# Kernel tuning notes

Hardware: AMD Instinct MI355X
Metric: run time of the kernel (lower is better)

## Reference

```python
import jax, jax.numpy as jnp
import numpy as np

NV = 20000; NC = 20000; E = 500000
IN_SHAPE = 2; PE_DIM = 8; HID = 64; NL = 3
EPS = 1e-7  # GENConv message eps


def _lin(x, w, b):
    return x @ w + b


def _encode(x, pe, ew, eb, pw1, pb1, pw2, pb2):
    # relu(cat([Linear(x), 0.5*(pe_mlp(pe)+pe_mlp(-pe))], dim=1))
    def pe_mlp(p):
        return _lin(jax.nn.relu(_lin(p, pw1, pb1)), pw2, pb2)
    h = jnp.concatenate([_lin(x, ew, eb), 0.5 * (pe_mlp(pe) + pe_mlp(-pe))], axis=1)
    return jax.nn.relu(h)


def _genconv(x_src, x_dst, src, dst, ewt, lew, leb, w1, b1, w2, b2, n_dst):
    # GENConv(aggr='softmax', t=1, norm=None, msg_norm=False, edge_dim=1)
    msg = jax.nn.relu(x_src[src] + _lin(ewt, lew, leb)) + EPS  # [E, HID]
    m = jax.ops.segment_max(msg, dst, num_segments=n_dst)      # stable segment softmax
    ex = jnp.exp(msg - m[dst])
    s = jax.ops.segment_sum(ex, dst, num_segments=n_dst)
    agg = jax.ops.segment_sum(ex / (s[dst] + 1e-16) * msg, dst, num_segments=n_dst)
    out = agg + x_dst
    return _lin(jax.nn.relu(_lin(out, w1, b1)), w2, b2)  # MLP [hid -> 2hid -> hid]


def setup_inputs() -> dict:
    key = jax.random.key(0)
    ks = iter(jax.random.split(key, 64))
    d = {}
    d['x_vals'] = jax.random.normal(next(ks), (NV, IN_SHAPE), jnp.float32)
    d['x_cons'] = jax.random.normal(next(ks), (NC, IN_SHAPE), jnp.float32)
    d['pe_vals'] = jax.random.normal(next(ks), (NV, PE_DIM), jnp.float32)
    d['pe_cons'] = jax.random.normal(next(ks), (NC, PE_DIM), jnp.float32)
    d['edge_index_v2c'] = jnp.stack([
        jax.random.randint(next(ks), (E,), 0, NV),
        jax.random.randint(next(ks), (E,), 0, NC)])
    d['edge_index_c2v'] = jnp.stack([
        jax.random.randint(next(ks), (E,), 0, NC),
        jax.random.randint(next(ks), (E,), 0, NV)])
    d['edge_weight_v2c'] = jax.random.normal(next(ks), (E, 1), jnp.float32)
    d['edge_weight_c2v'] = jax.random.normal(next(ks), (E, 1), jnp.float32)
    def p(shape):
        return jax.random.normal(next(ks), shape, jnp.float32) * 0.05
    for k_ in ['vals', 'cons']:
        d[f'enc_{k_}_w'] = p((IN_SHAPE, HID // 2)); d[f'enc_{k_}_b'] = p((HID // 2,))
        d[f'pe_{k_}_w1'] = p((PE_DIM, HID)); d[f'pe_{k_}_b1'] = p((HID,))
        d[f'pe_{k_}_w2'] = p((HID, HID // 2)); d[f'pe_{k_}_b2'] = p((HID // 2,))
    for c in ['v2c', 'c2v']:
        d[f'{c}_edge_w'] = p((NL, 1, HID)); d[f'{c}_edge_b'] = p((NL, HID))
        d[f'{c}_w1'] = p((NL, HID, 2 * HID)); d[f'{c}_b1'] = p((NL, 2 * HID))
        d[f'{c}_w2'] = p((NL, 2 * HID, HID)); d[f'{c}_b2'] = p((NL, HID))
    for k_ in ['vals', 'cons']:
        d[f'pred_{k_}_w1'] = p((HID, HID)); d[f'pred_{k_}_b1'] = p((HID,))
        d[f'pred_{k_}_w2'] = p((HID, 1)); d[f'pred_{k_}_b2'] = p((1,))
    return d


def reference(x_vals, x_cons, pe_vals, pe_cons, edge_index_v2c, edge_index_c2v,
              edge_weight_v2c, edge_weight_c2v,
              enc_vals_w, enc_vals_b, pe_vals_w1, pe_vals_b1, pe_vals_w2, pe_vals_b2,
              enc_cons_w, enc_cons_b, pe_cons_w1, pe_cons_b1, pe_cons_w2, pe_cons_b2,
              v2c_edge_w, v2c_edge_b, v2c_w1, v2c_b1, v2c_w2, v2c_b2,
              c2v_edge_w, c2v_edge_b, c2v_w1, c2v_b1, c2v_w2, c2v_b2,
              pred_vals_w1, pred_vals_b1, pred_vals_w2, pred_vals_b2,
              pred_cons_w1, pred_cons_b1, pred_cons_w2, pred_cons_b2):
    vals = _encode(x_vals, pe_vals, enc_vals_w, enc_vals_b,
                   pe_vals_w1, pe_vals_b1, pe_vals_w2, pe_vals_b2)
    cons = _encode(x_cons, pe_cons, enc_cons_w, enc_cons_b,
                   pe_cons_w1, pe_cons_b1, pe_cons_w2, pe_cons_b2)
    hv, hc = [], []
    for i in range(NL):
        cons = _genconv(vals, cons, edge_index_v2c[0], edge_index_v2c[1],
                        edge_weight_v2c, v2c_edge_w[i], v2c_edge_b[i],
                        v2c_w1[i], v2c_b1[i], v2c_w2[i], v2c_b2[i], NC)
        vals = _genconv(cons, vals, edge_index_c2v[0], edge_index_c2v[1],
                        edge_weight_c2v, c2v_edge_w[i], c2v_edge_b[i],
                        c2v_w1[i], c2v_b1[i], c2v_w2[i], c2v_b2[i], NV)
        hc.append(cons); hv.append(vals)
    V = jnp.stack(hv)  # [NL, NV, HID]
    C = jnp.stack(hc)  # [NL, NC, HID]
    pv = _lin(jax.nn.relu(_lin(V, pred_vals_w1, pred_vals_b1)), pred_vals_w2, pred_vals_b2)
    pc = _lin(jax.nn.relu(_lin(C, pred_cons_w1, pred_cons_b1)), pred_cons_w2, pred_cons_b2)
    return pv[..., 0].T, pc[..., 0].T  # [NV, NL], [NC, NL]
```

## Files before the change

### kernel.cpp

```cpp
#include <hip/hip_runtime.h>
#include <hip/hip_fp16.h>

#define NVN 20000
#define NCN 20000
#define NE  500000
#define HID 64
#define NLAYER 3
#define TN 40
#define BSH 8
#define NB 79
#define CAPSH 14
#define CAP (1 << CAPSH)
#define NBCAP (NB * CAP)
#define P1E 2048

__device__ __forceinline__ float relu_(float x) { return fmaxf(x, 0.0f); }

__global__ __launch_bounds__(256) void bininit_kernel(
    int* __restrict__ bincurA, int* __restrict__ bincurB)
{
    int t = threadIdx.x;
    if (t < NB) { bincurA[t] = t << CAPSH; bincurB[t] = t << CAPSH; }
}

__global__ __launch_bounds__(256) void scatter_p1_kernel(
    const int* __restrict__ eiA, const float* __restrict__ ewA,
    int* __restrict__ bincurA, int2* __restrict__ stageA,
    const int* __restrict__ eiB, const float* __restrict__ ewB,
    int* __restrict__ bincurB, int2* __restrict__ stageB)
{
    __shared__ int rnk[P1E];
    __shared__ int cnt[NB], base_[NB];
    int t = threadIdx.x;
    int e0 = blockIdx.x * P1E;

    for (int g = 0; g < 2; ++g) {
        const int* ei   = g ? eiB : eiA;
        const float* ew = g ? ewB : ewA;
        int* bincur     = g ? bincurB : bincurA;
        int2* stage     = g ? stageB : stageA;

        if (t < NB) cnt[t] = 0;
        __syncthreads();
        for (int i = t; i < P1E; i += 256) {
            int e = e0 + i;
            if (e < NE) {
                int d = ei[NE + e];
                rnk[i] = atomicAdd(&cnt[d >> BSH], 1);
            }
        }
        __syncthreads();
        if (t < NB && cnt[t] > 0) base_[t] = atomicAdd(&bincur[t], cnt[t]);
        __syncthreads();
        for (int i = t; i < P1E; i += 256) {
            int e = e0 + i;
            if (e < NE) {
                int s = ei[e], d = ei[NE + e];
                float w = ew[e];
                stage[base_[d >> BSH] + rnk[i]] =
                    make_int2((int)((unsigned)s | ((unsigned)d << 16)), __float_as_int(w));
            }
        }
        __syncthreads();
    }
}

__global__ __launch_bounds__(1024) void scatter_p2_kernel(
    const int* __restrict__ bincurA, const int2* __restrict__ stageA,
    int* __restrict__ rowptrA, int* __restrict__ rowendA, int2* __restrict__ pairA,
    const int* __restrict__ bincurB, const int2* __restrict__ stageB,
    int* __restrict__ rowptrB, int* __restrict__ rowendB, int2* __restrict__ pairB)
{
    __shared__ int deg[256], pfx[256], cur[256];
    int g = blockIdx.x / NB;
    int b = blockIdx.x % NB;
    const int* bincur  = g ? bincurB : bincurA;
    const int2* stage  = g ? stageB : stageA;
    int* rowptr        = g ? rowptrB : rowptrA;
    int* rowend        = g ? rowendB : rowendA;
    int2* pair         = g ? pairB : pairA;

    int d0 = b << BSH;
    int d1 = min(d0 + 256, NCN);
    int nd = d1 - d0;
    int t = threadIdx.x;
    int estart = b << CAPSH;
    int eend = bincur[b];

    if (t < 256) deg[t] = 0;
    __syncthreads();
    for (int e = estart + t; e < eend; e += 1024) {
        int dst = (int)((unsigned)stage[e].x >> 16);
        atomicAdd(&deg[dst - d0], 1);
    }
    __syncthreads();
    if (t < 256) pfx[t] = deg[t];
    __syncthreads();
    for (int off = 1; off < 256; off <<= 1) {
        int v = (t >= off && t < 256) ? pfx[t - off] : 0;
        __syncthreads();
        if (t < 256) pfx[t] += v;
        __syncthreads();
    }
    if (t < nd) {
        int ex = estart + pfx[t] - deg[t];
        rowptr[d0 + t] = ex;
        rowend[d0 + t] = estart + pfx[t];
        cur[t] = ex;
    }
    __syncthreads();
    for (int e = estart + t; e < eend; e += 1024) {
        int2 s = stage[e];
        unsigned u = (unsigned)s.x;
        int src = (int)(u & 0xFFFFu);
        int dst = (int)(u >> 16);
        int p = atomicAdd(&cur[dst - d0], 1);
        pair[p] = make_int2(src, s.y);
    }
}

__global__ __launch_bounds__(256) void encode2_kernel(
    const float* __restrict__ xv, const float* __restrict__ pev,
    const float* __restrict__ ewv, const float* __restrict__ ebv,
    const float* __restrict__ pw1v, const float* __restrict__ pb1v,
    const float* __restrict__ pw2v, const float* __restrict__ pb2v,
    const float* __restrict__ xc, const float* __restrict__ pec,
    const float* __restrict__ ewc, const float* __restrict__ ebc,
    const float* __restrict__ pw1c, const float* __restrict__ pb1c,
    const float* __restrict__ pw2c, const float* __restrict__ pb2c,
    float* __restrict__ outv, float* __restrict__ outc,
    __half* __restrict__ outv16, __half* __restrict__ outc16)
{
    __shared__ float sh[4][64];
    const int VB = (NVN + 3) / 4;
    int wave = threadIdx.x >> 6, lane = threadIdx.x & 63;
    int b = blockIdx.x;
    bool isC = (b >= VB);
    const float* x   = isC ? xc : xv;
    const float* pe  = isC ? pec : pev;
    const float* ew  = isC ? ewc : ewv;
    const float* eb  = isC ? ebc : ebv;
    const float* pw1 = isC ? pw1c : pw1v;
    const float* pb1 = isC ? pb1c : pb1v;
    const float* pw2 = isC ? pw2c : pw2v;
    const float* pb2 = isC ? pb2c : pb2v;
    float* out = isC ? outc : outv;
    __half* out16 = isC ? outc16 : outv16;
    int N = isC ? NCN : NVN;
    int n = (isC ? b - VB : b) * 4 + wave;
    if (n >= N) return;

    float accp = pb1[lane], accm = accp;
#pragma unroll
    for (int k = 0; k < 8; ++k) {
        float p = pe[n * 8 + k];
        float w = pw1[k * 64 + lane];
        accp += p * w;
        accm -= p * w;
    }
    float hs = 0.5f * (relu_(accp) + relu_(accm));
    float* my = sh[wave];
    my[lane] = hs;
    __builtin_amdgcn_wave_barrier();

    int col = lane & 31;
    float peo = pb2[col];
#pragma unroll
    for (int k = 0; k < 64; k += 4) {
        float4 hv = *(const float4*)(my + k);
        peo = fmaf(hv.x, pw2[(k + 0) * 32 + col], peo);
        peo = fmaf(hv.y, pw2[(k + 1) * 32 + col], peo);
        peo = fmaf(hv.z, pw2[(k + 2) * 32 + col], peo);
        peo = fmaf(hv.w, pw2[(k + 3) * 32 + col], peo);
    }
    float lino = x[n * 2 + 0] * ew[col] + x[n * 2 + 1] * ew[32 + col] + eb[col];
    float h = (lane < 32) ? lino : peo;
    float r = relu_(h);
    out[n * 64 + lane] = r;
    out16[n * 64 + lane] = __float2half(r);
}

__global__ __launch_bounds__(256, 8) void edge_agg_kernel(
    const __half* __restrict__ xsrc,
    const float* __restrict__ xdst,
    const int* __restrict__ rowptr,
    const int* __restrict__ rowend,
    const int2* __restrict__ pair,
    const float* __restrict__ lew,
    const float* __restrict__ leb,
    float* __restrict__ oa,
    int N)
{
    int wave = threadIdx.x >> 6, lane = threadIdx.x & 63;
    int n = blockIdx.x * 4 + wave;
    if (n >= N) return;

    int start = __builtin_amdgcn_readfirstlane(rowptr[n]);
    int end   = __builtin_amdgcn_readfirstlane(rowend[n]);
    float lw = lew[lane], lb = leb[lane];
    float xd = xdst[(size_t)n * 64 + lane];

    float den = 0.0f, num = 0.0f;
    int j = start;

    if (j + 8 <= end) {
        int2 pb[8];
#pragma unroll
        for (int c = 0; c < 8; ++c) pb[c] = pair[j + c];

        for (; j + 16 <= end; j += 8) {
            float xv[8];
#pragma unroll
            for (int c = 0; c < 8; ++c)
                xv[c] = __half2float(xsrc[(size_t)pb[c].x * 64 + lane]);
            int2 pn[8];
#pragma unroll
            for (int c = 0; c < 8; ++c) pn[c] = pair[j + 8 + c];
#pragma unroll
            for (int c = 0; c < 8; ++c) {
                float msg = relu_(fmaf(__int_as_float(pb[c].y), lw, xv[c] + lb)) + 1e-7f;
                float e = __expf(msg);
                den += e;
                num = fmaf(e, msg, num);
            }
#pragma unroll
            for (int c = 0; c < 8; ++c) pb[c] = pn[c];
        }
        {
            float xv[8];
#pragma unroll
            for (int c = 0; c < 8; ++c)
                xv[c] = __half2float(xsrc[(size_t)pb[c].x * 64 + lane]);
#pragma unroll
            for (int c = 0; c < 8; ++c) {
                float msg = relu_(fmaf(__int_as_float(pb[c].y), lw, xv[c] + lb)) + 1e-7f;
                float e = __expf(msg);
                den += e;
                num = fmaf(e, msg, num);
            }
            j += 8;
        }
    }
    for (; j < end; ++j) {
        int2 p = pair[j];
        float xv = __half2float(xsrc[(size_t)p.x * 64 + lane]);
        float msg = relu_(fmaf(__int_as_float(p.y), lw, xv + lb)) + 1e-7f;
        float e = __expf(msg);
        den += e;
        num = fmaf(e, msg, num);
    }

    oa[(size_t)n * 64 + lane] = num / (den + 1e-16f) + xd;
}

__global__ __launch_bounds__(256, 4) void mlp_kernel(
    const float* __restrict__ oa,
    float* __restrict__ feat,
    __half* __restrict__ feat16,
    const float* __restrict__ w1,
    const float* __restrict__ b1,
    const float* __restrict__ w2,
    const float* __restrict__ b2,
    const float* __restrict__ pw1,
    const float* __restrict__ pb1,
    const float* __restrict__ pw2,
    const float* __restrict__ pb2,
    float* __restrict__ outp,
    int N, int layer)
{
    __shared__ float act[TN][68];
    __shared__ float hid[TN][132];
    __shared__ float b1s[128];
    __shared__ float b2s[64];
    __shared__ float pb1s[64];
    __shared__ float pw2s[64];

    int tid = threadIdx.x;
    if (tid < 128) b1s[tid] = b1[tid];
    if (tid < 64) { b2s[tid] = b2[tid]; pb1s[tid] = pb1[tid]; pw2s[tid] = pw2[tid]; }
    float pb2v = pb2[0];

    int o4 = (tid & 31) * 4;
    int o2 = (tid & 31) * 2;
    int n5 = (tid >> 5) * 5;
    __syncthreads();

    int ntiles = N / TN;
    for (int tile = blockIdx.x; tile < ntiles; tile += gridDim.x) {
        int base = tile * TN;
        {
            const float4* g4 = (const float4*)(oa + (size_t)base * 64);
            for (int i = tid; i < TN * 16; i += 256)
                *(float4*)&act[i >> 4][(i & 15) * 4] = g4[i];
        }
        __syncthreads();

        {
            float acc[5][4];
#pragma unroll
            for (int i = 0; i < 5; ++i)
#pragma unroll
                for (int q = 0; q < 4; ++q) acc[i][q] = b1s[o4 + q];
#pragma unroll 2
            for (int k = 0; k < 64; k += 4) {
                float4 a[5];
#pragma unroll
                for (int i = 0; i < 5; ++i) a[i] = *(const float4*)&act[n5 + i][k];
                float4 w0 = *(const float4*)&w1[(k + 0) * 128 + o4];
                float4 wq1 = *(const float4*)&w1[(k + 1) * 128 + o4];
                float4 wq2 = *(const float4*)&w1[(k + 2) * 128 + o4];
                float4 wq3 = *(const float4*)&w1[(k + 3) * 128 + o4];
#pragma unroll
                for (int i = 0; i < 5; ++i) {
                    acc[i][0] = fmaf(a[i].x, w0.x, acc[i][0]);
                    acc[i][1] = fmaf(a[i].x, w0.y, acc[i][1]);
                    acc[i][2] = fmaf(a[i].x, w0.z, acc[i][2]);
                    acc[i][3] = fmaf(a[i].x, w0.w, acc[i][3]);
                    acc[i][0] = fmaf(a[i].y, wq1.x, acc[i][0]);
                    acc[i][1] = fmaf(a[i].y, wq1.y, acc[i][1]);
                    acc[i][2] = fmaf(a[i].y, wq1.z, acc[i][2]);
                    acc[i][3] = fmaf(a[i].y, wq1.w, acc[i][3]);
                    acc[i][0] = fmaf(a[i].z, wq2.x, acc[i][0]);
                    acc[i][1] = fmaf(a[i].z, wq2.y, acc[i][1]);
                    acc[i][2] = fmaf(a[i].z, wq2.z, acc[i][2]);
                    acc[i][3] = fmaf(a[i].z, wq2.w, acc[i][3]);
                    acc[i][0] = fmaf(a[i].w, wq3.x, acc[i][0]);
                    acc[i][1] = fmaf(a[i].w, wq3.y, acc[i][1]);
                    acc[i][2] = fmaf(a[i].w, wq3.z, acc[i][2]);
                    acc[i][3] = fmaf(a[i].w, wq3.w, acc[i][3]);
                }
            }
#pragma unroll
            for (int i = 0; i < 5; ++i) {
                float4 h4 = make_float4(relu_(acc[i][0]), relu_(acc[i][1]),
                                        relu_(acc[i][2]), relu_(acc[i][3]));
                *(float4*)&hid[n5 + i][o4] = h4;
            }
        }
        __syncthreads();

        {
            float acc[5][2];
#pragma unroll
            for (int i = 0; i < 5; ++i) { acc[i][0] = b2s[o2]; acc[i][1] = b2s[o2 + 1]; }
#pragma unroll 2
            for (int k = 0; k < 128; k += 4) {
                float4 a[5];
#pragma unroll
                for (int i = 0; i < 5; ++i) a[i] = *(const float4*)&hid[n5 + i][k];
                float2 w0 = *(const float2*)&w2[(k + 0) * 64 + o2];
                float2 wq1 = *(const float2*)&w2[(k + 1) * 64 + o2];
                float2 wq2 = *(const float2*)&w2[(k + 2) * 64 + o2];
                float2 wq3 = *(const float2*)&w2[(k + 3) * 64 + o2];
#pragma unroll
                for (int i = 0; i < 5; ++i) {
                    acc[i][0] = fmaf(a[i].x, w0.x, acc[i][0]);
                    acc[i][1] = fmaf(a[i].x, w0.y, acc[i][1]);
                    acc[i][0] = fmaf(a[i].y, wq1.x, acc[i][0]);
                    acc[i][1] = fmaf(a[i].y, wq1.y, acc[i][1]);
                    acc[i][0] = fmaf(a[i].z, wq2.x, acc[i][0]);
                    acc[i][1] = fmaf(a[i].z, wq2.y, acc[i][1]);
                    acc[i][0] = fmaf(a[i].w, wq3.x, acc[i][0]);
                    acc[i][1] = fmaf(a[i].w, wq3.y, acc[i][1]);
                }
            }
#pragma unroll
            for (int i = 0; i < 5; ++i) {
                float2 r2 = make_float2(acc[i][0], acc[i][1]);
                *(float2*)&feat[(size_t)(base + n5 + i) * 64 + o2] = r2;
                *(__half2*)&feat16[(size_t)(base + n5 + i) * 64 + o2] =
                    __floats2half2_rn(r2.x, r2.y);
                *(float2*)&act[n5 + i][o2] = r2;
            }
        }
        __syncthreads();

        {
            float acc[5][2];
#pragma unroll
            for (int i = 0; i < 5; ++i) { acc[i][0] = pb1s[o2]; acc[i][1] = pb1s[o2 + 1]; }
#pragma unroll 2
            for (int k = 0; k < 64; k += 4) {
                float4 a[5];
#pragma unroll
                for (int i = 0; i < 5; ++i) a[i] = *(const float4*)&act[n5 + i][k];
                float2 w0 = *(const float2*)&pw1[(k + 0) * 64 + o2];
                float2 wq1 = *(const float2*)&pw1[(k + 1) * 64 + o2];
                float2 wq2 = *(const float2*)&pw1[(k + 2) * 64 + o2];
                float2 wq3 = *(const float2*)&pw1[(k + 3) * 64 + o2];
#pragma unroll
                for (int i = 0; i < 5; ++i) {
                    acc[i][0] = fmaf(a[i].x, w0.x, acc[i][0]);
                    acc[i][1] = fmaf(a[i].x, w0.y, acc[i][1]);
                    acc[i][0] = fmaf(a[i].y, wq1.x, acc[i][0]);
                    acc[i][1] = fmaf(a[i].y, wq1.y, acc[i][1]);
                    acc[i][0] = fmaf(a[i].z, wq2.x, acc[i][0]);
                    acc[i][1] = fmaf(a[i].z, wq2.y, acc[i][1]);
                    acc[i][0] = fmaf(a[i].w, wq3.x, acc[i][0]);
                    acc[i][1] = fmaf(a[i].w, wq3.y, acc[i][1]);
                }
            }
            float pw2a = pw2s[o2], pw2b = pw2s[o2 + 1];
            float ps[5];
#pragma unroll
            for (int i = 0; i < 5; ++i)
                ps[i] = relu_(acc[i][0]) * pw2a + relu_(acc[i][1]) * pw2b;
#pragma unroll
            for (int msk = 16; msk >= 1; msk >>= 1) {
#pragma unroll
                for (int i = 0; i < 5; ++i)
                    ps[i] += __shfl_xor(ps[i], msk, 64);
            }
            if ((tid & 31) == 0) {
#pragma unroll
                for (int i = 0; i < 5; ++i)
                    outp[(size_t)(base + n5 + i) * NLAYER + layer] = ps[i] + pb2v;
            }
        }
        __syncthreads();
    }
}

extern "C" void kernel_launch(void* const* d_in, const int* in_sizes, int n_in,
                              void* d_out, int out_size, void* d_ws, size_t ws_size,
                              hipStream_t stream)
{
    const float* x_vals   = (const float*)d_in[0];
    const float* x_cons   = (const float*)d_in[1];
    const float* pe_vals  = (const float*)d_in[2];
    const float* pe_cons  = (const float*)d_in[3];
    const int*   ei_v2c   = (const int*)d_in[4];
    const int*   ei_c2v   = (const int*)d_in[5];
    const float* ew_v2c   = (const float*)d_in[6];
    const float* ew_c2v   = (const float*)d_in[7];
    const float* enc_vals_w = (const float*)d_in[8];
    const float* enc_vals_b = (const float*)d_in[9];
    const float* pe_vals_w1 = (const float*)d_in[10];
    const float* pe_vals_b1 = (const float*)d_in[11];
    const float* pe_vals_w2 = (const float*)d_in[12];
    const float* pe_vals_b2 = (const float*)d_in[13];
    const float* enc_cons_w = (const float*)d_in[14];
    const float* enc_cons_b = (const float*)d_in[15];
    const float* pe_cons_w1 = (const float*)d_in[16];
    const float* pe_cons_b1 = (const float*)d_in[17];
    const float* pe_cons_w2 = (const float*)d_in[18];
    const float* pe_cons_b2 = (const float*)d_in[19];
    const float* v2c_edge_w = (const float*)d_in[20];
    const float* v2c_edge_b = (const float*)d_in[21];
    const float* v2c_w1     = (const float*)d_in[22];
    const float* v2c_b1     = (const float*)d_in[23];
    const float* v2c_w2     = (const float*)d_in[24];
    const float* v2c_b2     = (const float*)d_in[25];
    const float* c2v_edge_w = (const float*)d_in[26];
    const float* c2v_edge_b = (const float*)d_in[27];
    const float* c2v_w1     = (const float*)d_in[28];
    const float* c2v_b1     = (const float*)d_in[29];
    const float* c2v_w2     = (const float*)d_in[30];
    const float* c2v_b2     = (const float*)d_in[31];
    const float* pred_vals_w1 = (const float*)d_in[32];
    const float* pred_vals_b1 = (const float*)d_in[33];
    const float* pred_vals_w2 = (const float*)d_in[34];
    const float* pred_vals_b2 = (const float*)d_in[35];
    const float* pred_cons_w1 = (const float*)d_in[36];
    const float* pred_cons_b1 = (const float*)d_in[37];
    const float* pred_cons_w2 = (const float*)d_in[38];
    const float* pred_cons_b2 = (const float*)d_in[39];

    float* out = (float*)d_out;
    float* out_c = out + (size_t)NVN * NLAYER;

    const size_t NF = (size_t)NVN * 64;

    float* ws     = (float*)d_ws;
    float* feat_v = ws;
    float* feat_c = feat_v + NF;
    float* oa     = feat_c + NF;
    int2* v2c_pair  = (int2*)(oa + NF);
    int2* c2v_pair  = v2c_pair + NBCAP;
    int2* v2c_stage = c2v_pair + NBCAP;
    int2* c2v_stage = v2c_stage + NBCAP;
    __half* feat16_v = (__half*)(c2v_stage + NBCAP);
    __half* feat16_c = feat16_v + NF;
    int* ip = (int*)(feat16_c + NF);
    int* v2c_bincur  = ip; ip += NB;
    int* c2v_bincur  = ip; ip += NB;
    int* v2c_rowptr  = ip; ip += NCN;
    int* v2c_rowend  = ip; ip += NCN;
    int* c2v_rowptr  = ip; ip += NVN;
    int* c2v_rowend  = ip; ip += NVN;

    const int p1b = (NE + P1E - 1) / P1E;

    bininit_kernel<<<1, 256, 0, stream>>>(v2c_bincur, c2v_bincur);
    scatter_p1_kernel<<<p1b, 256, 0, stream>>>(
        ei_v2c, ew_v2c, v2c_bincur, v2c_stage,
        ei_c2v, ew_c2v, c2v_bincur, c2v_stage);
    scatter_p2_kernel<<<2 * NB, 1024, 0, stream>>>(
        v2c_bincur, v2c_stage, v2c_rowptr, v2c_rowend, v2c_pair,
        c2v_bincur, c2v_stage, c2v_rowptr, c2v_rowend, c2v_pair);

    encode2_kernel<<<(NVN + 3) / 4 + (NCN + 3) / 4, 256, 0, stream>>>(
        x_vals, pe_vals, enc_vals_w, enc_vals_b,
        pe_vals_w1, pe_vals_b1, pe_vals_w2, pe_vals_b2,
        x_cons, pe_cons, enc_cons_w, enc_cons_b,
        pe_cons_w1, pe_cons_b1, pe_cons_w2, pe_cons_b2,
        feat_v, feat_c, feat16_v, feat16_c);

    for (int i = 0; i < NLAYER; ++i) {
        edge_agg_kernel<<<(NCN + 3) / 4, 256, 0, stream>>>(
            feat16_v, feat_c, v2c_rowptr, v2c_rowend, v2c_pair,
            v2c_edge_w + (size_t)i * HID, v2c_edge_b + (size_t)i * HID,
            oa, NCN);
        mlp_kernel<<<NCN / TN, 256, 0, stream>>>(
            oa, feat_c, feat16_c,
            v2c_w1 + (size_t)i * 8192, v2c_b1 + (size_t)i * 128,
            v2c_w2 + (size_t)i * 8192, v2c_b2 + (size_t)i * 64,
            pred_cons_w1, pred_cons_b1, pred_cons_w2, pred_cons_b2,
            out_c, NCN, i);
        edge_agg_kernel<<<(NVN + 3) / 4, 256, 0, stream>>>(
            feat16_c, feat_v, c2v_rowptr, c2v_rowend, c2v_pair,
            c2v_edge_w + (size_t)i * HID, c2v_edge_b + (size_t)i * HID,
            oa, NVN);
        mlp_kernel<<<NVN / TN, 256, 0, stream>>>(
            oa, feat_v, feat16_v,
            c2v_w1 + (size_t)i * 8192, c2v_b1 + (size_t)i * 128,
            c2v_w2 + (size_t)i * 8192, c2v_b2 + (size_t)i * 64,
            pred_vals_w1, pred_vals_b1, pred_vals_w2, pred_vals_b2,
            out, NVN, i);
    }
}
```

Measured before the change: 426.0 us.

## Fuse edge softmax aggregation with node MLP into a single kernel

Each block now aggregates the incoming edges of 8 destination nodes, keeps the aggregated rows in shared memory, and runs the two-layer MLP plus the prediction head on them in the same kernel. This removes the global round trip through the intermediate `oa` buffer and halves the number of kernel launches per layer. In exchange, the MLP tile shrinks from 40 to 8 nodes, so each weight element is reused across fewer rows and more weight traffic goes through the caches.

```diff
diff --git a/kernel.cpp b/kernel.cpp
--- a/kernel.cpp
+++ b/kernel.cpp
@@ -6,7 +6,7 @@
 #define NE  500000
 #define HID 64
 #define NLAYER 3
-#define TN 40
+#define TN 8
 #define BSH 8
 #define NB 79
 #define CAPSH 14
@@ -180,7 +180,7 @@
     out16[n * 64 + lane] = __float2half(r);
 }
 
-__global__ __launch_bounds__(256, 8) void edge_agg_kernel(
+__global__ __launch_bounds__(256, 8) void fused_kernel(
     const __half* __restrict__ xsrc,
     const float* __restrict__ xdst,
     const int* __restrict__ rowptr,
@@ -188,73 +188,6 @@
     const int2* __restrict__ pair,
     const float* __restrict__ lew,
     const float* __restrict__ leb,
-    float* __restrict__ oa,
-    int N)
-{
-    int wave = threadIdx.x >> 6, lane = threadIdx.x & 63;
-    int n = blockIdx.x * 4 + wave;
-    if (n >= N) return;
-
-    int start = __builtin_amdgcn_readfirstlane(rowptr[n]);
-    int end   = __builtin_amdgcn_readfirstlane(rowend[n]);
-    float lw = lew[lane], lb = leb[lane];
-    float xd = xdst[(size_t)n * 64 + lane];
-
-    float den = 0.0f, num = 0.0f;
-    int j = start;
-
-    if (j + 8 <= end) {
-        int2 pb[8];
-#pragma unroll
-        for (int c = 0; c < 8; ++c) pb[c] = pair[j + c];
-
-        for (; j + 16 <= end; j += 8) {
-            float xv[8];
-#pragma unroll
-            for (int c = 0; c < 8; ++c)
-                xv[c] = __half2float(xsrc[(size_t)pb[c].x * 64 + lane]);
-            int2 pn[8];
-#pragma unroll
-            for (int c = 0; c < 8; ++c) pn[c] = pair[j + 8 + c];
-#pragma unroll
-            for (int c = 0; c < 8; ++c) {
-                float msg = relu_(fmaf(__int_as_float(pb[c].y), lw, xv[c] + lb)) + 1e-7f;
-                float e = __expf(msg);
-                den += e;
-                num = fmaf(e, msg, num);
-            }
-#pragma unroll
-            for (int c = 0; c < 8; ++c) pb[c] = pn[c];
-        }
-        {
-            float xv[8];
-#pragma unroll
-            for (int c = 0; c < 8; ++c)
-                xv[c] = __half2float(xsrc[(size_t)pb[c].x * 64 + lane]);
-#pragma unroll
-            for (int c = 0; c < 8; ++c) {
-                float msg = relu_(fmaf(__int_as_float(pb[c].y), lw, xv[c] + lb)) + 1e-7f;
-                float e = __expf(msg);
-                den += e;
-                num = fmaf(e, msg, num);
-            }
-            j += 8;
-        }
-    }
-    for (; j < end; ++j) {
-        int2 p = pair[j];
-        float xv = __half2float(xsrc[(size_t)p.x * 64 + lane]);
-        float msg = relu_(fmaf(__int_as_float(p.y), lw, xv + lb)) + 1e-7f;
-        float e = __expf(msg);
-        den += e;
-        num = fmaf(e, msg, num);
-    }
-
-    oa[(size_t)n * 64 + lane] = num / (den + 1e-16f) + xd;
-}
-
-__global__ __launch_bounds__(256, 4) void mlp_kernel(
-    const float* __restrict__ oa,
     float* __restrict__ feat,
     __half* __restrict__ feat16,
     const float* __restrict__ w1,
@@ -270,154 +203,163 @@
 {
     __shared__ float act[TN][68];
     __shared__ float hid[TN][132];
-    __shared__ float b1s[128];
-    __shared__ float b2s[64];
-    __shared__ float pb1s[64];
-    __shared__ float pw2s[64];
 
     int tid = threadIdx.x;
-    if (tid < 128) b1s[tid] = b1[tid];
-    if (tid < 64) { b2s[tid] = b2[tid]; pb1s[tid] = pb1[tid]; pw2s[tid] = pw2[tid]; }
-    float pb2v = pb2[0];
+    int wave = tid >> 6, lane = tid & 63;
+    int base = blockIdx.x * TN;
+
+    {
+        float lw = lew[lane], lb = leb[lane];
+#pragma unroll
+        for (int q = 0; q < 2; ++q) {
+            int row = wave * 2 + q;
+            int n = base + row;
+            int start = __builtin_amdgcn_readfirstlane(rowptr[n]);
+            int end   = __builtin_amdgcn_readfirstlane(rowend[n]);
+            float xd = xdst[(size_t)n * 64 + lane];
+
+            float den = 0.0f, num = 0.0f;
+            int j = start;
+
+            if (j + 8 <= end) {
+                int2 pb[8];
+#pragma unroll
+                for (int c = 0; c < 8; ++c) pb[c] = pair[j + c];
+
+                for (; j + 16 <= end; j += 8) {
+                    float xv[8];
+#pragma unroll
+                    for (int c = 0; c < 8; ++c)
+                        xv[c] = __half2float(xsrc[(size_t)pb[c].x * 64 + lane]);
+                    int2 pn[8];
+#pragma unroll
+                    for (int c = 0; c < 8; ++c) pn[c] = pair[j + 8 + c];
+#pragma unroll
+                    for (int c = 0; c < 8; ++c) {
+                        float msg = relu_(fmaf(__int_as_float(pb[c].y), lw, xv[c] + lb)) + 1e-7f;
+                        float e = __expf(msg);
+                        den += e;
+                        num = fmaf(e, msg, num);
+                    }
+#pragma unroll
+                    for (int c = 0; c < 8; ++c) pb[c] = pn[c];
+                }
+                {
+                    float xv[8];
+#pragma unroll
+                    for (int c = 0; c < 8; ++c)
+                        xv[c] = __half2float(xsrc[(size_t)pb[c].x * 64 + lane]);
+#pragma unroll
+                    for (int c = 0; c < 8; ++c) {
+                        float msg = relu_(fmaf(__int_as_float(pb[c].y), lw, xv[c] + lb)) + 1e-7f;
+                        float e = __expf(msg);
+                        den += e;
+                        num = fmaf(e, msg, num);
+                    }
+                    j += 8;
+                }
+            }
+            for (; j < end; ++j) {
+                int2 p = pair[j];
+                float xv = __half2float(xsrc[(size_t)p.x * 64 + lane]);
+                float msg = relu_(fmaf(__int_as_float(p.y), lw, xv + lb)) + 1e-7f;
+                float e = __expf(msg);
+                den += e;
+                num = fmaf(e, msg, num);
+            }
+
+            act[row][lane] = num / (den + 1e-16f) + xd;
+        }
+    }
+    __syncthreads();
 
     int o4 = (tid & 31) * 4;
     int o2 = (tid & 31) * 2;
-    int n5 = (tid >> 5) * 5;
-    __syncthreads();
-
-    int ntiles = N / TN;
-    for (int tile = blockIdx.x; tile < ntiles; tile += gridDim.x) {
-        int base = tile * TN;
-        {
-            const float4* g4 = (const float4*)(oa + (size_t)base * 64);
-            for (int i = tid; i < TN * 16; i += 256)
-                *(float4*)&act[i >> 4][(i & 15) * 4] = g4[i];
-        }
-        __syncthreads();
-
-        {
-            float acc[5][4];
-#pragma unroll
-            for (int i = 0; i < 5; ++i)
-#pragma unroll
-                for (int q = 0; q < 4; ++q) acc[i][q] = b1s[o4 + q];
+    int node = tid >> 5;
+
+    {
+        float4 bb = *(const float4*)&b1[o4];
+        float acc0 = bb.x, acc1 = bb.y, acc2 = bb.z, acc3 = bb.w;
 #pragma unroll 2
-            for (int k = 0; k < 64; k += 4) {
-                float4 a[5];
-#pragma unroll
-                for (int i = 0; i < 5; ++i) a[i] = *(const float4*)&act[n5 + i][k];
-                float4 w0 = *(const float4*)&w1[(k + 0) * 128 + o4];
-                float4 wq1 = *(const float4*)&w1[(k + 1) * 128 + o4];
-                float4 wq2 = *(const float4*)&w1[(k + 2) * 128 + o4];
-                float4 wq3 = *(const float4*)&w1[(k + 3) * 128 + o4];
-#pragma unroll
-                for (int i = 0; i < 5; ++i) {
-                    acc[i][0] = fmaf(a[i].x, w0.x, acc[i][0]);
-                    acc[i][1] = fmaf(a[i].x, w0.y, acc[i][1]);
-                    acc[i][2] = fmaf(a[i].x, w0.z, acc[i][2]);
-                    acc[i][3] = fmaf(a[i].x, w0.w, acc[i][3]);
-                    acc[i][0] = fmaf(a[i].y, wq1.x, acc[i][0]);
-                    acc[i][1] = fmaf(a[i].y, wq1.y, acc[i][1]);
-                    acc[i][2] = fmaf(a[i].y, wq1.z, acc[i][2]);
-                    acc[i][3] = fmaf(a[i].y, wq1.w, acc[i][3]);
-                    acc[i][0] = fmaf(a[i].z, wq2.x, acc[i][0]);
-                    acc[i][1] = fmaf(a[i].z, wq2.y, acc[i][1]);
-                    acc[i][2] = fmaf(a[i].z, wq2.z, acc[i][2]);
-                    acc[i][3] = fmaf(a[i].z, wq2.w, acc[i][3]);
-                    acc[i][0] = fmaf(a[i].w, wq3.x, acc[i][0]);
-                    acc[i][1] = fmaf(a[i].w, wq3.y, acc[i][1]);
-                    acc[i][2] = fmaf(a[i].w, wq3.z, acc[i][2]);
-                    acc[i][3] = fmaf(a[i].w, wq3.w, acc[i][3]);
-                }
-            }
-#pragma unroll
-            for (int i = 0; i < 5; ++i) {
-                float4 h4 = make_float4(relu_(acc[i][0]), relu_(acc[i][1]),
-                                        relu_(acc[i][2]), relu_(acc[i][3]));
-                *(float4*)&hid[n5 + i][o4] = h4;
-            }
-        }
-        __syncthreads();
-
-        {
-            float acc[5][2];
-#pragma unroll
-            for (int i = 0; i < 5; ++i) { acc[i][0] = b2s[o2]; acc[i][1] = b2s[o2 + 1]; }
+        for (int k = 0; k < 64; k += 4) {
+            float4 a = *(const float4*)&act[node][k];
+            float4 w0 = *(const float4*)&w1[(k + 0) * 128 + o4];
+            float4 wq1 = *(const float4*)&w1[(k + 1) * 128 + o4];
+            float4 wq2 = *(const float4*)&w1[(k + 2) * 128 + o4];
+            float4 wq3 = *(const float4*)&w1[(k + 3) * 128 + o4];
+            acc0 = fmaf(a.x, w0.x, acc0);
+            acc1 = fmaf(a.x, w0.y, acc1);
+            acc2 = fmaf(a.x, w0.z, acc2);
+            acc3 = fmaf(a.x, w0.w, acc3);
+            acc0 = fmaf(a.y, wq1.x, acc0);
+            acc1 = fmaf(a.y, wq1.y, acc1);
+            acc2 = fmaf(a.y, wq1.z, acc2);
+            acc3 = fmaf(a.y, wq1.w, acc3);
+            acc0 = fmaf(a.z, wq2.x, acc0);
+            acc1 = fmaf(a.z, wq2.y, acc1);
+            acc2 = fmaf(a.z, wq2.z, acc2);
+            acc3 = fmaf(a.z, wq2.w, acc3);
+            acc0 = fmaf(a.w, wq3.x, acc0);
+            acc1 = fmaf(a.w, wq3.y, acc1);
+            acc2 = fmaf(a.w, wq3.z, acc2);
+            acc3 = fmaf(a.w, wq3.w, acc3);
+        }
+        *(float4*)&hid[node][o4] = make_float4(relu_(acc0), relu_(acc1),
+                                               relu_(acc2), relu_(acc3));
+    }
+    __syncthreads();
+
+    {
+        float2 bb = *(const float2*)&b2[o2];
+        float acc0 = bb.x, acc1 = bb.y;
 #pragma unroll 2
-            for (int k = 0; k < 128; k += 4) {
-                float4 a[5];
-#pragma unroll
-                for (int i = 0; i < 5; ++i) a[i] = *(const float4*)&hid[n5 + i][k];
-                float2 w0 = *(const float2*)&w2[(k + 0) * 64 + o2];
-                float2 wq1 = *(const float2*)&w2[(k + 1) * 64 + o2];
-                float2 wq2 = *(const float2*)&w2[(k + 2) * 64 + o2];
-                float2 wq3 = *(const float2*)&w2[(k + 3) * 64 + o2];
-#pragma unroll
-                for (int i = 0; i < 5; ++i) {
-                    acc[i][0] = fmaf(a[i].x, w0.x, acc[i][0]);
-                    acc[i][1] = fmaf(a[i].x, w0.y, acc[i][1]);
-                    acc[i][0] = fmaf(a[i].y, wq1.x, acc[i][0]);
-                    acc[i][1] = fmaf(a[i].y, wq1.y, acc[i][1]);
-                    acc[i][0] = fmaf(a[i].z, wq2.x, acc[i][0]);
-                    acc[i][1] = fmaf(a[i].z, wq2.y, acc[i][1]);
-                    acc[i][0] = fmaf(a[i].w, wq3.x, acc[i][0]);
-                    acc[i][1] = fmaf(a[i].w, wq3.y, acc[i][1]);
-                }
-            }
-#pragma unroll
-            for (int i = 0; i < 5; ++i) {
-                float2 r2 = make_float2(acc[i][0], acc[i][1]);
-                *(float2*)&feat[(size_t)(base + n5 + i) * 64 + o2] = r2;
-                *(__half2*)&feat16[(size_t)(base + n5 + i) * 64 + o2] =
-                    __floats2half2_rn(r2.x, r2.y);
-                *(float2*)&act[n5 + i][o2] = r2;
-            }
-        }
-        __syncthreads();
-
-        {
-            float acc[5][2];
-#pragma unroll
-            for (int i = 0; i < 5; ++i) { acc[i][0] = pb1s[o2]; acc[i][1] = pb1s[o2 + 1]; }
+        for (int k = 0; k < 128; k += 4) {
+            float4 a = *(const float4*)&hid[node][k];
+            float2 w0 = *(const float2*)&w2[(k + 0) * 64 + o2];
+            float2 wq1 = *(const float2*)&w2[(k + 1) * 64 + o2];
+            float2 wq2 = *(const float2*)&w2[(k + 2) * 64 + o2];
+            float2 wq3 = *(const float2*)&w2[(k + 3) * 64 + o2];
+            acc0 = fmaf(a.x, w0.x, acc0);
+            acc1 = fmaf(a.x, w0.y, acc1);
+            acc0 = fmaf(a.y, wq1.x, acc0);
+            acc1 = fmaf(a.y, wq1.y, acc1);
+            acc0 = fmaf(a.z, wq2.x, acc0);
+            acc1 = fmaf(a.z, wq2.y, acc1);
+            acc0 = fmaf(a.w, wq3.x, acc0);
+            acc1 = fmaf(a.w, wq3.y, acc1);
+        }
+        *(float2*)&feat[(size_t)(base + node) * 64 + o2] = make_float2(acc0, acc1);
+        *(__half2*)&feat16[(size_t)(base + node) * 64 + o2] = __floats2half2_rn(acc0, acc1);
+        *(float2*)&act[node][o2] = make_float2(acc0, acc1);
+    }
+    __syncthreads();
+
+    {
+        float2 bb = *(const float2*)&pb1[o2];
+        float acc0 = bb.x, acc1 = bb.y;
 #pragma unroll 2
-            for (int k = 0; k < 64; k += 4) {
-                float4 a[5];
-#pragma unroll
-                for (int i = 0; i < 5; ++i) a[i] = *(const float4*)&act[n5 + i][k];
-                float2 w0 = *(const float2*)&pw1[(k + 0) * 64 + o2];
-                float2 wq1 = *(const float2*)&pw1[(k + 1) * 64 + o2];
-                float2 wq2 = *(const float2*)&pw1[(k + 2) * 64 + o2];
-                float2 wq3 = *(const float2*)&pw1[(k + 3) * 64 + o2];
-#pragma unroll
-                for (int i = 0; i < 5; ++i) {
-                    acc[i][0] = fmaf(a[i].x, w0.x, acc[i][0]);
-                    acc[i][1] = fmaf(a[i].x, w0.y, acc[i][1]);
-                    acc[i][0] = fmaf(a[i].y, wq1.x, acc[i][0]);
-                    acc[i][1] = fmaf(a[i].y, wq1.y, acc[i][1]);
-                    acc[i][0] = fmaf(a[i].z, wq2.x, acc[i][0]);
-                    acc[i][1] = fmaf(a[i].z, wq2.y, acc[i][1]);
-                    acc[i][0] = fmaf(a[i].w, wq3.x, acc[i][0]);
-                    acc[i][1] = fmaf(a[i].w, wq3.y, acc[i][1]);
-                }
-            }
-            float pw2a = pw2s[o2], pw2b = pw2s[o2 + 1];
-            float ps[5];
-#pragma unroll
-            for (int i = 0; i < 5; ++i)
-                ps[i] = relu_(acc[i][0]) * pw2a + relu_(acc[i][1]) * pw2b;
-#pragma unroll
-            for (int msk = 16; msk >= 1; msk >>= 1) {
-#pragma unroll
-                for (int i = 0; i < 5; ++i)
-                    ps[i] += __shfl_xor(ps[i], msk, 64);
-            }
-            if ((tid & 31) == 0) {
-#pragma unroll
-                for (int i = 0; i < 5; ++i)
-                    outp[(size_t)(base + n5 + i) * NLAYER + layer] = ps[i] + pb2v;
-            }
-        }
-        __syncthreads();
+        for (int k = 0; k < 64; k += 4) {
+            float4 a = *(const float4*)&act[node][k];
+            float2 w0 = *(const float2*)&pw1[(k + 0) * 64 + o2];
+            float2 wq1 = *(const float2*)&pw1[(k + 1) * 64 + o2];
+            float2 wq2 = *(const float2*)&pw1[(k + 2) * 64 + o2];
+            float2 wq3 = *(const float2*)&pw1[(k + 3) * 64 + o2];
+            acc0 = fmaf(a.x, w0.x, acc0);
+            acc1 = fmaf(a.x, w0.y, acc1);
+            acc0 = fmaf(a.y, wq1.x, acc0);
+            acc1 = fmaf(a.y, wq1.y, acc1);
+            acc0 = fmaf(a.z, wq2.x, acc0);
+            acc1 = fmaf(a.z, wq2.y, acc1);
+            acc0 = fmaf(a.w, wq3.x, acc0);
+            acc1 = fmaf(a.w, wq3.y, acc1);
+        }
+        float2 pwv = *(const float2*)&pw2[o2];
+        float ps = relu_(acc0) * pwv.x + relu_(acc1) * pwv.y;
+#pragma unroll
+        for (int msk = 16; msk >= 1; msk >>= 1)
+            ps += __shfl_xor(ps, msk, 64);
+        if ((tid & 31) == 0)
+            outp[(size_t)(base + node) * NLAYER + layer] = ps + pb2[0];
     }
 }
 
@@ -507,22 +449,18 @@
         feat_v, feat_c, feat16_v, feat16_c);
 
     for (int i = 0; i < NLAYER; ++i) {
-        edge_agg_kernel<<<(NCN + 3) / 4, 256, 0, stream>>>(
+        fused_kernel<<<NCN / TN, 256, 0, stream>>>(
             feat16_v, feat_c, v2c_rowptr, v2c_rowend, v2c_pair,
             v2c_edge_w + (size_t)i * HID, v2c_edge_b + (size_t)i * HID,
-            oa, NCN);
-        mlp_kernel<<<NCN / TN, 256, 0, stream>>>(
-            oa, feat_c, feat16_c,
+            feat_c, feat16_c,
             v2c_w1 + (size_t)i * 8192, v2c_b1 + (size_t)i * 128,
             v2c_w2 + (size_t)i * 8192, v2c_b2 + (size_t)i * 64,
             pred_cons_w1, pred_cons_b1, pred_cons_w2, pred_cons_b2,
             out_c, NCN, i);
-        edge_agg_kernel<<<(NVN + 3) / 4, 256, 0, stream>>>(
+        fused_kernel<<<NVN / TN, 256, 0, stream>>>(
             feat16_c, feat_v, c2v_rowptr, c2v_rowend, c2v_pair,
             c2v_edge_w + (size_t)i * HID, c2v_edge_b + (size_t)i * HID,
-            oa, NVN);
-        mlp_kernel<<<NVN / TN, 256, 0, stream>>>(
-            oa, feat_v, feat16_v,
+            feat_v, feat16_v,
             c2v_w1 + (size_t)i * 8192, c2v_b1 + (size_t)i * 128,
             c2v_w2 + (size_t)i * 8192, c2v_b2 + (size_t)i * 64,
             pred_vals_w1, pred_vals_b1, pred_vals_w2, pred_vals_b2,
```

After: 694.1 us. +62.9%, slower.

## Defer prediction head to single batched kernel using layer feature snapshots

Applied to the files above, without the earlier changes.

Removes the prediction-head MLP from the per-layer mlp_kernel. Intermediate layer features are instead written to snapshot buffers that reuse the staging workspace, and one pred_kernel computes all layers and both sides at the end. This shortens the per-layer kernels on the critical path and batches the prediction work into a single launch with more parallelism. The cost is extra global writes for the snapshots and re-reading the features later.

```diff
diff --git a/kernel.cpp b/kernel.cpp
--- a/kernel.cpp
+++ b/kernel.cpp
@@ -13,6 +13,8 @@
 #define CAP (1 << CAPSH)
 #define NBCAP (NB * CAP)
 #define P1E 2048
+#define NTILES (NVN / TN)
+#define SNAPL (NLAYER - 1)
 
 __device__ __forceinline__ float relu_(float x) { return fmaxf(x, 0.0f); }
 
@@ -257,28 +259,21 @@
     const float* __restrict__ oa,
     float* __restrict__ feat,
     __half* __restrict__ feat16,
+    float* __restrict__ snap,
     const float* __restrict__ w1,
     const float* __restrict__ b1,
     const float* __restrict__ w2,
     const float* __restrict__ b2,
-    const float* __restrict__ pw1,
-    const float* __restrict__ pb1,
-    const float* __restrict__ pw2,
-    const float* __restrict__ pb2,
-    float* __restrict__ outp,
-    int N, int layer)
+    int N)
 {
     __shared__ float act[TN][68];
     __shared__ float hid[TN][132];
     __shared__ float b1s[128];
     __shared__ float b2s[64];
-    __shared__ float pb1s[64];
-    __shared__ float pw2s[64];
 
     int tid = threadIdx.x;
     if (tid < 128) b1s[tid] = b1[tid];
-    if (tid < 64) { b2s[tid] = b2[tid]; pb1s[tid] = pb1[tid]; pw2s[tid] = pw2[tid]; }
-    float pb2v = pb2[0];
+    if (tid < 64) b2s[tid] = b2[tid];
 
     int o4 = (tid & 31) * 4;
     int o2 = (tid & 31) * 2;
@@ -367,57 +362,101 @@
 #pragma unroll
             for (int i = 0; i < 5; ++i) {
                 float2 r2 = make_float2(acc[i][0], acc[i][1]);
-                *(float2*)&feat[(size_t)(base + n5 + i) * 64 + o2] = r2;
-                *(__half2*)&feat16[(size_t)(base + n5 + i) * 64 + o2] =
-                    __floats2half2_rn(r2.x, r2.y);
-                *(float2*)&act[n5 + i][o2] = r2;
-            }
-        }
-        __syncthreads();
-
-        {
-            float acc[5][2];
-#pragma unroll
-            for (int i = 0; i < 5; ++i) { acc[i][0] = pb1s[o2]; acc[i][1] = pb1s[o2 + 1]; }
+                size_t off = (size_t)(base + n5 + i) * 64 + o2;
+                *(float2*)&feat[off] = r2;
+                if (snap) *(float2*)&snap[off] = r2;
+                *(__half2*)&feat16[off] = __floats2half2_rn(r2.x, r2.y);
+            }
+        }
+        __syncthreads();
+    }
+}
+
+__global__ __launch_bounds__(256, 4) void pred_kernel(
+    const float* __restrict__ snap,
+    const float* __restrict__ featv,
+    const float* __restrict__ featc,
+    const float* __restrict__ pv_w1, const float* __restrict__ pv_b1,
+    const float* __restrict__ pv_w2, const float* __restrict__ pv_b2,
+    const float* __restrict__ pc_w1, const float* __restrict__ pc_b1,
+    const float* __restrict__ pc_w2, const float* __restrict__ pc_b2,
+    float* __restrict__ out)
+{
+    __shared__ float act[TN][68];
+    __shared__ float pb1s[64];
+    __shared__ float pw2s[64];
+
+    int bid = blockIdx.x;
+    int side  = bid / (NLAYER * NTILES);
+    int rem   = bid % (NLAYER * NTILES);
+    int layer = rem / NTILES;
+    int tile  = rem % NTILES;
+
+    const float* pw1 = side ? pc_w1 : pv_w1;
+    const float* pb1 = side ? pc_b1 : pv_b1;
+    const float* pw2 = side ? pc_w2 : pv_w2;
+    const float* pb2 = side ? pc_b2 : pv_b2;
+    const float* src;
+    if (layer == NLAYER - 1)
+        src = side ? featc : featv;
+    else
+        src = snap + ((size_t)side * SNAPL + layer) * ((size_t)NVN * 64);
+    float* outp = out + (size_t)side * NVN * NLAYER;
+
+    int tid = threadIdx.x;
+    if (tid < 64) { pb1s[tid] = pb1[tid]; pw2s[tid] = pw2[tid]; }
+    float pb2v = pb2[0];
+
+    int o2 = (tid & 31) * 2;
+    int n5 = (tid >> 5) * 5;
+    int base = tile * TN;
+
+    {
+        const float4* g4 = (const float4*)(src + (size_t)base * 64);
+        for (int i = tid; i < TN * 16; i += 256)
+            *(float4*)&act[i >> 4][(i & 15) * 4] = g4[i];
+    }
+    __syncthreads();
+
+    float acc[5][2];
+#pragma unroll
+    for (int i = 0; i < 5; ++i) { acc[i][0] = pb1s[o2]; acc[i][1] = pb1s[o2 + 1]; }
 #pragma unroll 2
-            for (int k = 0; k < 64; k += 4) {
-                float4 a[5];
-#pragma unroll
-                for (int i = 0; i < 5; ++i) a[i] = *(const float4*)&act[n5 + i][k];
-                float2 w0 = *(const float2*)&pw1[(k + 0) * 64 + o2];
-                float2 wq1 = *(const float2*)&pw1[(k + 1) * 64 + o2];
-                float2 wq2 = *(const float2*)&pw1[(k + 2) * 64 + o2];
-                float2 wq3 = *(const float2*)&pw1[(k + 3) * 64 + o2];
-#pragma unroll
-                for (int i = 0; i < 5; ++i) {
-                    acc[i][0] = fmaf(a[i].x, w0.x, acc[i][0]);
-                    acc[i][1] = fmaf(a[i].x, w0.y, acc[i][1]);
-                    acc[i][0] = fmaf(a[i].y, wq1.x, acc[i][0]);
-                    acc[i][1] = fmaf(a[i].y, wq1.y, acc[i][1]);
-                    acc[i][0] = fmaf(a[i].z, wq2.x, acc[i][0]);
-                    acc[i][1] = fmaf(a[i].z, wq2.y, acc[i][1]);
-                    acc[i][0] = fmaf(a[i].w, wq3.x, acc[i][0]);
-                    acc[i][1] = fmaf(a[i].w, wq3.y, acc[i][1]);
-                }
-            }
-            float pw2a = pw2s[o2], pw2b = pw2s[o2 + 1];
-            float ps[5];
-#pragma unroll
-            for (int i = 0; i < 5; ++i)
-                ps[i] = relu_(acc[i][0]) * pw2a + relu_(acc[i][1]) * pw2b;
-#pragma unroll
-            for (int msk = 16; msk >= 1; msk >>= 1) {
-#pragma unroll
-                for (int i = 0; i < 5; ++i)
-                    ps[i] += __shfl_xor(ps[i], msk, 64);
-            }
-            if ((tid & 31) == 0) {
-#pragma unroll
-                for (int i = 0; i < 5; ++i)
-                    outp[(size_t)(base + n5 + i) * NLAYER + layer] = ps[i] + pb2v;
-            }
-        }
-        __syncthreads();
+    for (int k = 0; k < 64; k += 4) {
+        float4 a[5];
+#pragma unroll
+        for (int i = 0; i < 5; ++i) a[i] = *(const float4*)&act[n5 + i][k];
+        float2 w0 = *(const float2*)&pw1[(k + 0) * 64 + o2];
+        float2 wq1 = *(const float2*)&pw1[(k + 1) * 64 + o2];
+        float2 wq2 = *(const float2*)&pw1[(k + 2) * 64 + o2];
+        float2 wq3 = *(const float2*)&pw1[(k + 3) * 64 + o2];
+#pragma unroll
+        for (int i = 0; i < 5; ++i) {
+            acc[i][0] = fmaf(a[i].x, w0.x, acc[i][0]);
+            acc[i][1] = fmaf(a[i].x, w0.y, acc[i][1]);
+            acc[i][0] = fmaf(a[i].y, wq1.x, acc[i][0]);
+            acc[i][1] = fmaf(a[i].y, wq1.y, acc[i][1]);
+            acc[i][0] = fmaf(a[i].z, wq2.x, acc[i][0]);
+            acc[i][1] = fmaf(a[i].z, wq2.y, acc[i][1]);
+            acc[i][0] = fmaf(a[i].w, wq3.x, acc[i][0]);
+            acc[i][1] = fmaf(a[i].w, wq3.y, acc[i][1]);
+        }
+    }
+    float pw2a = pw2s[o2], pw2b = pw2s[o2 + 1];
+    float ps[5];
+#pragma unroll
+    for (int i = 0; i < 5; ++i)
+        ps[i] = relu_(acc[i][0]) * pw2a + relu_(acc[i][1]) * pw2b;
+#pragma unroll
+    for (int msk = 16; msk >= 1; msk >>= 1) {
+#pragma unroll
+        for (int i = 0; i < 5; ++i)
+            ps[i] += __shfl_xor(ps[i], msk, 64);
+    }
+    if ((tid & 31) == 0) {
+#pragma unroll
+        for (int i = 0; i < 5; ++i)
+            outp[(size_t)(base + n5 + i) * NLAYER + layer] = ps[i] + pb2v;
     }
 }
 
@@ -467,7 +506,6 @@
     const float* pred_cons_b2 = (const float*)d_in[39];
 
     float* out = (float*)d_out;
-    float* out_c = out + (size_t)NVN * NLAYER;
 
     const size_t NF = (size_t)NVN * 64;
 
@@ -479,6 +517,7 @@
     int2* c2v_pair  = v2c_pair + NBCAP;
     int2* v2c_stage = c2v_pair + NBCAP;
     int2* c2v_stage = v2c_stage + NBCAP;
+    float* snap = (float*)v2c_stage;
     __half* feat16_v = (__half*)(c2v_stage + NBCAP);
     __half* feat16_c = feat16_v + NF;
     int* ip = (int*)(feat16_c + NF);
@@ -507,25 +546,31 @@
         feat_v, feat_c, feat16_v, feat16_c);
 
     for (int i = 0; i < NLAYER; ++i) {
+        float* snap_c = (i < SNAPL) ? snap + ((size_t)SNAPL + i) * NF : nullptr;
+        float* snap_v = (i < SNAPL) ? snap + (size_t)i * NF : nullptr;
         edge_agg_kernel<<<(NCN + 3) / 4, 256, 0, stream>>>(
             feat16_v, feat_c, v2c_rowptr, v2c_rowend, v2c_pair,
             v2c_edge_w + (size_t)i * HID, v2c_edge_b + (size_t)i * HID,
             oa, NCN);
         mlp_kernel<<<NCN / TN, 256, 0, stream>>>(
-            oa, feat_c, feat16_c,
+            oa, feat_c, feat16_c, snap_c,
             v2c_w1 + (size_t)i * 8192, v2c_b1 + (size_t)i * 128,
             v2c_w2 + (size_t)i * 8192, v2c_b2 + (size_t)i * 64,
-            pred_cons_w1, pred_cons_b1, pred_cons_w2, pred_cons_b2,
-            out_c, NCN, i);
+            NCN);
         edge_agg_kernel<<<(NVN + 3) / 4, 256, 0, stream>>>(
             feat16_c, feat_v, c2v_rowptr, c2v_rowend, c2v_pair,
             c2v_edge_w + (size_t)i * HID, c2v_edge_b + (size_t)i * HID,
             oa, NVN);
         mlp_kernel<<<NVN / TN, 256, 0, stream>>>(
-            oa, feat_v, feat16_v,
+            oa, feat_v, feat16_v, snap_v,
             c2v_w1 + (size_t)i * 8192, c2v_b1 + (size_t)i * 128,
             c2v_w2 + (size_t)i * 8192, c2v_b2 + (size_t)i * 64,
-            pred_vals_w1, pred_vals_b1, pred_vals_w2, pred_vals_b2,
-            out, NVN, i);
-    }
-}
+            NVN);
+    }
+
+    pred_kernel<<<2 * NLAYER * NTILES, 256, 0, stream>>>(
+        snap, feat_v, feat_c,
+        pred_vals_w1, pred_vals_b1, pred_vals_w2, pred_vals_b2,
+        pred_cons_w1, pred_cons_b1, pred_cons_w2, pred_cons_b2,
+        out);
+}
```

New measurement: 423.5 us, median of 2. Within noise of the previous version (-0.6%).
